# Optimization experiments

Measured on AMD Instinct MI355X. Metric: run time of the kernel, lower is better.

Reference implementation:

```python
import jax, jax.numpy as jnp
import numpy as np

HEADS = 16
D_MODEL = 1024
D_K = D_MODEL // HEADS
B, S = 2, 2048
NEG = -1000000000.0


def setup_inputs() -> dict:
    key = jax.random.key(0)
    ks = jax.random.split(key, 8)
    q = jax.random.normal(ks[0], (B, S, D_MODEL), dtype=jnp.float32)
    k = jax.random.normal(ks[1], (B, S, D_MODEL), dtype=jnp.float32)
    v = jax.random.normal(ks[2], (B, S, D_MODEL), dtype=jnp.float32)
    mask = jax.random.randint(ks[3], (B, 1, S, S), 0, 2) > 0  # True = masked
    scale = 1.0 / np.sqrt(D_MODEL)
    Wq = jax.random.normal(ks[4], (D_MODEL, D_MODEL), dtype=jnp.float32) * scale
    Wk = jax.random.normal(ks[5], (D_MODEL, D_MODEL), dtype=jnp.float32) * scale
    Wv = jax.random.normal(ks[6], (D_MODEL, D_MODEL), dtype=jnp.float32) * scale
    Wo = jax.random.normal(ks[7], (D_MODEL, D_MODEL), dtype=jnp.float32) * scale
    return {"q": q, "k": k, "v": v, "mask": mask,
            "Wq": Wq, "Wk": Wk, "Wv": Wv, "Wo": Wo}


def reference(q, k, v, mask, Wq, Wk, Wv, Wo):
    b, s, _ = q.shape
    # torch Linear: x @ W.T ; reshape to [B, H, S, d_k]
    def proj(x, W):
        return (x @ W.T).reshape(b, -1, HEADS, D_K).transpose(0, 2, 1, 3)
    qh, kh, vh = proj(q, Wq), proj(k, Wk), proj(v, Wv)
    # scaled dot-product attention; scale uses d_k (key.shape[-1] after reshape)
    att = jnp.einsum('bhqd,bhkd->bhqk', qh, kh) / jnp.sqrt(jnp.float32(D_K))
    att = jnp.where(mask, NEG, att)
    att = jax.nn.softmax(att, axis=-1)
    out = jnp.einsum('bhqk,bhkd->bhqd', att, vh)  # [B,H,S,d_k]
    out = out.transpose(0, 2, 1, 3).reshape(b, -1, D_MODEL)
    return out @ Wo.T  # dropout is identity at inference
```

## Files before the change

kernel.cpp:

```cpp
#include <hip/hip_runtime.h>

typedef unsigned short u16;
typedef unsigned int   u32;
typedef unsigned char  u8;
typedef unsigned long long u64;
typedef __attribute__((ext_vector_type(8))) short bf16x8;
typedef __attribute__((ext_vector_type(4))) float f32x4;
typedef __attribute__((ext_vector_type(16))) float f32x16;

__device__ __forceinline__ u16 f2b(float f) {
  union { float f; u32 u; } v; v.f = f;
  u32 u = v.u;
  return (u16)((u + 0x7fffu + ((u >> 16) & 1u)) >> 16);
}
__device__ __forceinline__ float b2f(u16 x) {
  union { u32 u; float f; } v; v.u = ((u32)x) << 16; return v.f;
}
__device__ __forceinline__ u32 pk2(u16 lo, u16 hi) { return (u32)lo | ((u32)hi << 16); }

__device__ __forceinline__ float fexp2(float x) { return __builtin_amdgcn_exp2f(x); }

__device__ __forceinline__ u32 cvtpk(float lo, float hi) {
  u32 r;
  asm("v_cvt_pk_bf16_f32 %0, %1, %2" : "=v"(r) : "v"(lo), "v"(hi));
  return r;
}

__device__ __forceinline__ void swap32(u32& a, u32& b) {
  asm("v_permlane32_swap_b32 %0, %1" : "+v"(a), "+v"(b));
}

__device__ __forceinline__ void glds16(const u16* g, u16* l) {
  __builtin_amdgcn_global_load_lds((const __attribute__((address_space(1))) void*)g,
                                   (__attribute__((address_space(3))) void*)l, 16, 0, 0);
}

__global__ __launch_bounds__(256) void mask_detect(const u8* __restrict__ raw,
                                                   int* __restrict__ flag) {
  int i = blockIdx.x * 256 + threadIdx.x;
  uint4 x = ((const uint4*)raw)[i];
  u32 o = x.x | x.y | x.z | x.w;
  u64 b1 = __ballot((o & 0x0000ff00u) != 0);
  u64 b2 = __ballot((o & 0xffff0000u) != 0);
  if ((threadIdx.x & 63) == 0) {
    if (b1) atomicOr(&flag[0], 1);
    if (b2) atomicOr(&flag[1], 1);
  }
}

__global__ __launch_bounds__(256) void mask_bits(const u8* __restrict__ raw,
                                                 u64* __restrict__ out,
                                                 const int* __restrict__ flag) {
  int f = flag[0] ? 2 : (flag[1] ? 1 : 0);
  int i = blockIdx.x * 256 + threadIdx.x;
  bool bit;
  if (f == 2)      bit = raw[i] != 0;
  else if (f == 0) bit = ((const int*)raw)[i] != 0;
  else             bit = ((const float*)raw)[i] != 0.0f;
  u64 b = __ballot(bit);
  if ((threadIdx.x & 63) == 0) out[i >> 6] = b;
}

__global__ __launch_bounds__(256) void conv_all(
    const float* __restrict__ W0, const float* __restrict__ W1,
    const float* __restrict__ W2, const float* __restrict__ W3,
    const float* __restrict__ A0, const float* __restrict__ A1,
    const float* __restrict__ A2,
    u16* __restrict__ o0, u16* __restrict__ o1, u16* __restrict__ o2,
    u16* __restrict__ o3, u16* __restrict__ o4, u16* __restrict__ o5,
    u16* __restrict__ o6) {
  int gid = blockIdx.x * 256 + threadIdx.x;
  const float* src; u16* dst; int off;
  if (gid < 524288) {
    int wz = gid >> 17; off = (gid & 131071) * 8;
    src = wz == 0 ? W0 : wz == 1 ? W1 : wz == 2 ? W2 : W3;
    dst = wz == 0 ? o0 : wz == 1 ? o1 : wz == 2 ? o2 : o3;
  } else {
    int g2 = gid - 524288;
    int az = g2 >> 19; off = (g2 & 524287) * 8;
    src = az == 0 ? A0 : az == 1 ? A1 : A2;
    dst = az == 0 ? o4 : az == 1 ? o5 : o6;
  }
  float4 a = *(const float4*)(src + off), b2 = *(const float4*)(src + off + 4);
  uint4 t;
  t.x = pk2(f2b(a.x), f2b(a.y));   t.y = pk2(f2b(a.z), f2b(a.w));
  t.z = pk2(f2b(b2.x), f2b(b2.y)); t.w = pk2(f2b(b2.z), f2b(b2.w));
  *(uint4*)(dst + off) = t;
}

template<int CF32>
__device__ __forceinline__ void gemm_body(
    const u16* __restrict__ Av, const u16* __restrict__ Bv, void* __restrict__ Cv,
    int N, int K, int m0, int n0, float cscale, u16* As, u16* Bs) {
  const int tid = threadIdx.x;
  const int lane = tid & 63, w = tid >> 6;
  const int lr = lane & 15, lg = lane >> 4;
  const int wm = (w >> 1) * 64, wn = (w & 1) * 64;
  const int srow = lane >> 3;
  const int selem = (((lane & 7) ^ srow) << 3);
  const int rsw = (lr & 7) << 3;

  f32x4 acc[4][4];
#pragma unroll
  for (int mi = 0; mi < 4; ++mi)
#pragma unroll
    for (int ni = 0; ni < 4; ++ni)
      acc[mi][ni] = (f32x4){0.f, 0.f, 0.f, 0.f};

#define GSTAGE(buf, k0_)                                                       \
  do {                                                                         \
    _Pragma("unroll")                                                          \
    for (int r_ = 0; r_ < 4; ++r_) {                                           \
      const int c_ = w * 4 + r_;                                               \
      const int row_ = c_ * 8 + srow;                                          \
      glds16(Av + (size_t)(m0 + row_) * K + (k0_) + selem, As + (buf) * 8192 + c_ * 512); \
      glds16(Bv + (size_t)(n0 + row_) * K + (k0_) + selem, Bs + (buf) * 8192 + c_ * 512); \
    }                                                                          \
  } while (0)

  GSTAGE(0, 0);
  __syncthreads();
  int cur = 0;
  for (int k0 = 0; k0 < K; k0 += 64) {
    if (k0 + 64 < K) GSTAGE(cur ^ 1, k0 + 64);
    bf16x8 af[4][2], bfv[4][2];
#pragma unroll
    for (int mi = 0; mi < 4; ++mi)
#pragma unroll
      for (int kk = 0; kk < 2; ++kk)
        af[mi][kk] = *(bf16x8*)&As[cur * 8192 + (wm + mi * 16 + lr) * 64 + ((kk * 32 + lg * 8) ^ rsw)];
#pragma unroll
    for (int ni = 0; ni < 4; ++ni)
#pragma unroll
      for (int kk = 0; kk < 2; ++kk)
        bfv[ni][kk] = *(bf16x8*)&Bs[cur * 8192 + (wn + ni * 16 + lr) * 64 + ((kk * 32 + lg * 8) ^ rsw)];
    __builtin_amdgcn_s_setprio(1);
#pragma unroll
    for (int mi = 0; mi < 4; ++mi)
#pragma unroll
      for (int ni = 0; ni < 4; ++ni)
#pragma unroll
        for (int kk = 0; kk < 2; ++kk)
          acc[mi][ni] = __builtin_amdgcn_mfma_f32_16x16x32_bf16(
              af[mi][kk], bfv[ni][kk], acc[mi][ni], 0, 0, 0);
    __builtin_amdgcn_s_setprio(0);
    __syncthreads();
    cur ^= 1;
  }
#undef GSTAGE
#pragma unroll
  for (int mi = 0; mi < 4; ++mi)
#pragma unroll
    for (int ni = 0; ni < 4; ++ni)
#pragma unroll
      for (int r = 0; r < 4; ++r) {
        int m = m0 + wm + mi * 16 + lg * 4 + r;
        int n = n0 + wn + ni * 16 + lr;
        float vv = acc[mi][ni][r] * cscale;
        if (CF32) ((float*)Cv)[(size_t)m * N + n] = vv;
        else      ((u16*)Cv)[(size_t)m * N + n] = f2b(vv);
      }
}

__global__ __launch_bounds__(256) void gemm_qkv(
    const u16* __restrict__ qb, const u16* __restrict__ kb, const u16* __restrict__ vb,
    const u16* __restrict__ Wqb, const u16* __restrict__ Wkb, const u16* __restrict__ Wvb,
    u16* __restrict__ Qb, u16* __restrict__ Kb, u16* __restrict__ VTb, float qscale) {
  __shared__ __align__(16) u16 As[2 * 8192];
  __shared__ __align__(16) u16 Bs[2 * 8192];
  const int z = blockIdx.z;
  const u16 *Av, *Bv; u16* Cv; int N, bxx, by; float cs = 1.0f;
  if (z < 2) {
    Av = z ? kb : qb; Bv = z ? Wkb : Wqb; Cv = z ? Kb : Qb;
    N = 1024; bxx = blockIdx.x & 7; by = blockIdx.x >> 3;
    if (!z) cs = qscale;
  } else {
    Av = Wvb; Bv = vb; Cv = VTb;
    N = 4096; bxx = blockIdx.x & 31; by = blockIdx.x >> 5;
  }
  gemm_body<0>(Av, Bv, Cv, N, 1024, by * 128, bxx * 128, cs, As, Bs);
}

__global__ __launch_bounds__(256) void gemm_o(
    const u16* __restrict__ Ob, const u16* __restrict__ Wob, float* __restrict__ C) {
  __shared__ __align__(16) u16 As[2 * 8192];
  __shared__ __align__(16) u16 Bs[2 * 8192];
  gemm_body<1>(Ob, Wob, C, 1024, 1024, blockIdx.y * 128, blockIdx.x * 128, 1.0f, As, Bs);
}

__global__ __launch_bounds__(256, 4) void flash12(const u16* __restrict__ Q,
                                                  const u16* __restrict__ K,
                                                  const u16* __restrict__ VT,
                                                  const u64* __restrict__ mpk,
                                                  u16* __restrict__ O0,
                                                  u16* __restrict__ O1,
                                                  u16* __restrict__ O2,
                                                  float* __restrict__ Lp) {
  __shared__ __align__(16) u16 Ks[2][4096];
  __shared__ __align__(16) u16 Vs[2][4096];
  const int tid = threadIdx.x, lane = tid & 63, w = tid >> 6;
  const int c = lane & 31, h = lane >> 5;
  const int bid = blockIdx.x;
  const int xcd = bid & 7, idx = bid >> 3;
  const int gl = idx >> 4, qblk = idx & 15;
  const int group = xcd * 12 + gl;
  const int split = group % 3;
  const int hb = group / 3;
  const int head = hb & 15, b = hb >> 4;
  const int qw = qblk * 128 + w * 32;
  const int kt0 = (split * 32) / 3;
  const int ktn = ((split + 1) * 32) / 3;
  const int nt = ktn - kt0;
  const size_t kbase = (size_t)b * 2048 * 1024 + (size_t)head * 64;
  const size_t vbase = (size_t)head * 64 * 4096 + (size_t)b * 2048;
  const int srow = lane >> 3;
  const int selem = (((lane & 7) ^ srow) << 3);
  const int rswc = (c & 7) << 3;

  bf16x8 qf[4];
#pragma unroll
  for (int kd = 0; kd < 4; ++kd)
    qf[kd] = *(const bf16x8*)&Q[kbase + (size_t)(qw + c) * 1024 + 16 * kd + 8 * h];

  union { u32 u[4]; bf16x8 v; } ones;
#pragma unroll
  for (int i = 0; i < 4; ++i) ones.u[i] = 0x3f803f80u;

  f32x16 accO0, accO1, accL;
#pragma unroll
  for (int i = 0; i < 16; ++i) { accO0[i] = 0.f; accO1[i] = 0.f; accL[i] = 0.f; }

  const u64* mrp = mpk + ((size_t)b * 2048 + qw + c) * 32;

#define STAGE(buf, t)                                                          \
  do {                                                                         \
    const int k0_ = (t) * 64;                                                  \
    _Pragma("unroll")                                                          \
    for (int r_ = 0; r_ < 2; ++r_) {                                           \
      const int c_ = w * 2 + r_;                                               \
      const int row_ = c_ * 8 + srow;                                          \
      glds16(K + kbase + (size_t)(k0_ + row_) * 1024 + selem, &Ks[buf][c_ * 512]); \
    }                                                                          \
    _Pragma("unroll")                                                          \
    for (int r_ = 0; r_ < 2; ++r_) {                                           \
      const int c_ = w * 2 + r_;                                               \
      const int row_ = c_ * 8 + srow;                                          \
      glds16(VT + vbase + (size_t)row_ * 4096 + k0_ + selem, &Vs[buf][c_ * 512]); \
    }                                                                          \
  } while (0)

  STAGE(0, kt0);
  u64 mb_next = mrp[kt0];
  __syncthreads();

  int cur = 0;
  for (int t = 0; t < nt; ++t) {
    const u64 mb = mb_next;
    if (t + 1 < nt) {
      STAGE(cur ^ 1, kt0 + t + 1);
      mb_next = mrp[kt0 + t + 1];
    }
    const u16* ks = Ks[cur];
    const u16* vs = Vs[cur];
    f32x16 s0, s1;
#pragma unroll
    for (int i = 0; i < 16; ++i) { s0[i] = 0.f; s1[i] = 0.f; }
    __builtin_amdgcn_s_setprio(1);
#pragma unroll
    for (int kd = 0; kd < 4; ++kd) {
      bf16x8 kf0 = *(bf16x8*)&ks[c * 64 + ((16 * kd + 8 * h) ^ rswc)];
      s0 = __builtin_amdgcn_mfma_f32_32x32x16_bf16(kf0, qf[kd], s0, 0, 0, 0);
      bf16x8 kf1 = *(bf16x8*)&ks[(32 + c) * 64 + ((16 * kd + 8 * h) ^ rswc)];
      s1 = __builtin_amdgcn_mfma_f32_32x32x16_bf16(kf1, qf[kd], s1, 0, 0, 0);
    }
    __builtin_amdgcn_s_setprio(0);
    u32 pw[2][4][2];
#pragma unroll
    for (int kb = 0; kb < 2; ++kb) {
      const u32 m32 = (u32)(mb >> (32 * kb + 4 * h));
      float pp[16];
#pragma unroll
      for (int g = 0; g < 4; ++g)
#pragma unroll
        for (int r = 0; r < 4; ++r) {
          float e = fexp2(kb == 0 ? s0[4 * g + r] : s1[4 * g + r]);
          pp[4 * g + r] = ((m32 >> (8 * g + r)) & 1) ? 0.0f : e;
        }
#pragma unroll
      for (int g = 0; g < 4; ++g)
#pragma unroll
        for (int hh = 0; hh < 2; ++hh)
          pw[kb][g][hh] = cvtpk(pp[4 * g + 2 * hh], pp[4 * g + 2 * hh + 1]);
    }
    __builtin_amdgcn_s_setprio(1);
#pragma unroll
    for (int kb = 0; kb < 2; ++kb)
#pragma unroll
      for (int s = 0; s < 2; ++s) {
        u32 w0 = pw[kb][2 * s][0], w2 = pw[kb][2 * s + 1][0];
        swap32(w0, w2);
        u32 w1 = pw[kb][2 * s][1], w3 = pw[kb][2 * s + 1][1];
        swap32(w1, w3);
        union { u32 u[4]; bf16x8 v; } af;
        af.u[0] = w0; af.u[1] = w1; af.u[2] = w2; af.u[3] = w3;
        const int ksg = kb * 2 + s;
        bf16x8 vf0 = *(bf16x8*)&vs[c * 64 + ((16 * ksg + 8 * h) ^ rswc)];
        accO0 = __builtin_amdgcn_mfma_f32_32x32x16_bf16(af.v, vf0, accO0, 0, 0, 0);
        bf16x8 vf1 = *(bf16x8*)&vs[(32 + c) * 64 + ((16 * ksg + 8 * h) ^ rswc)];
        accO1 = __builtin_amdgcn_mfma_f32_32x32x16_bf16(af.v, vf1, accO1, 0, 0, 0);
        accL  = __builtin_amdgcn_mfma_f32_32x32x16_bf16(af.v, ones.v, accL, 0, 0, 0);
      }
    __builtin_amdgcn_s_setprio(0);
    __syncthreads();
    cur ^= 1;
  }
#undef STAGE
  u16* Op = split == 0 ? O0 : split == 1 ? O1 : O2;
  const size_t obase = (size_t)b * 2048 + qw;
#pragma unroll
  for (int g = 0; g < 4; ++g)
#pragma unroll
    for (int r = 0; r < 4; ++r) {
      const int qrow = r + 8 * g + 4 * h;
      const size_t row = obase + qrow;
      const size_t base = row * 1024 + (size_t)head * 64 + c;
      Op[base]      = f2b(accO0[4 * g + r]);
      Op[base + 32] = f2b(accO1[4 * g + r]);
      if (c == 0) Lp[(size_t)split * 65536 + row * 16 + head] = accL[4 * g + r];
    }
}

__global__ __launch_bounds__(256) void combine(const u16* __restrict__ O0,
                                               const u16* __restrict__ O1,
                                               const u16* __restrict__ O2,
                                               const float* __restrict__ Lp,
                                               u16* __restrict__ Ob) {
  int gid = blockIdx.x * 256 + threadIdx.x;
  int row = gid >> 7, chb = (gid & 127) * 8;
  int head = chb >> 6;
  float l = Lp[(size_t)row * 16 + head] + Lp[65536 + (size_t)row * 16 + head] +
            Lp[131072 + (size_t)row * 16 + head];
  float inv = 1.0f / l;
  size_t off = (size_t)row * 1024 + chb;
  union { uint4 q; u16 s[8]; } a, b, c2, o;
  a.q  = *(const uint4*)(O0 + off);
  b.q  = *(const uint4*)(O1 + off);
  c2.q = *(const uint4*)(O2 + off);
#pragma unroll
  for (int j = 0; j < 8; ++j)
    o.s[j] = f2b((b2f(a.s[j]) + b2f(b.s[j]) + b2f(c2.s[j])) * inv);
  *(uint4*)(Ob + off) = o.q;
}

extern "C" void kernel_launch(void* const* d_in, const int* in_sizes, int n_in,
                              void* d_out, int out_size, void* d_ws, size_t ws_size,
                              hipStream_t stream) {
  const float* q    = (const float*)d_in[0];
  const float* k    = (const float*)d_in[1];
  const float* v    = (const float*)d_in[2];
  const u8*    mask = (const u8*)d_in[3];
  const float* Wq   = (const float*)d_in[4];
  const float* Wk   = (const float*)d_in[5];
  const float* Wv   = (const float*)d_in[6];
  const float* Wo   = (const float*)d_in[7];

  u8* ws = (u8*)d_ws;
  int* flag = (int*)ws;
  u64* mpk  = (u64*)(ws + 256);
  u16* Wqb  = (u16*)(ws + 256 + (1u << 20));
  u16* Wkb  = Wqb + (1 << 20);
  u16* Wvb  = Wkb + (1 << 20);
  u16* Wob  = Wvb + (1 << 20);
  const size_t NE = (size_t)4096 * 1024;
  u16* vb   = Wob + (1 << 20);
  u16* O2   = vb;
  u16* Qb   = vb + NE;
  u16* Kb   = Qb + NE;
  u16* VTb  = Kb + NE;
  u16* qb   = (u16*)d_out;
  u16* kb   = qb + NE;
  u16* O0   = qb;
  u16* O1   = kb;
  float* Lp = (float*)Wqb;
  u16* Ob   = Qb;

  const float LOG2E = 1.4426950408889634f;

  hipMemsetAsync(flag, 0, 8, stream);
  mask_detect<<<32, 256, 0, stream>>>(mask, flag);
  mask_bits<<<32768, 256, 0, stream>>>(mask, mpk, flag);
  conv_all<<<8192, 256, 0, stream>>>(Wq, Wk, Wv, Wo, q, k, v,
                                     Wqb, Wkb, Wvb, Wob, qb, kb, vb);

  gemm_qkv<<<dim3(256, 1, 3), 256, 0, stream>>>(
      qb, kb, vb, Wqb, Wkb, Wvb, Qb, Kb, VTb, 0.125f * LOG2E);

  flash12<<<1536, 256, 0, stream>>>(Qb, Kb, VTb, mpk, O0, O1, O2, Lp);
  combine<<<2048, 256, 0, stream>>>(O0, O1, O2, Lp, Ob);

  gemm_o<<<dim3(8, 32), 256, 0, stream>>>(Ob, Wob, (float*)d_out);
}
```

Measured before the change: 162.9 us.

## Vectorize mask packing, single-buffer QKV GEMM, XCD-remap grids, 128x64 output GEMM

mask_bits now has each thread read 8 mask elements and write one packed byte, instead of using a ballot per element, so it launches 8x fewer blocks. The QKV GEMM switches to single-buffered LDS so more blocks fit per CU, and block indices are remapped so blocks sharing an operand land on the same XCD for L2 reuse. The output GEMM uses 128x64 tiles to get 512 blocks instead of 256, for better CU fill. The cost is losing the overlap between loads and compute in the single-buffered loops.

```diff
diff --git a/kernel.cpp b/kernel.cpp
--- a/kernel.cpp
+++ b/kernel.cpp
@@ -52,13 +52,25 @@
                                                  u64* __restrict__ out,
                                                  const int* __restrict__ flag) {
   int f = flag[0] ? 2 : (flag[1] ? 1 : 0);
-  int i = blockIdx.x * 256 + threadIdx.x;
-  bool bit;
-  if (f == 2)      bit = raw[i] != 0;
-  else if (f == 0) bit = ((const int*)raw)[i] != 0;
-  else             bit = ((const float*)raw)[i] != 0.0f;
-  u64 b = __ballot(bit);
-  if ((threadIdx.x & 63) == 0) out[i >> 6] = b;
+  int t = blockIdx.x * 256 + threadIdx.x;
+  u8 byte;
+  if (f == 2) {
+    u64 x = ((const u64*)raw)[t];
+    u64 nz = x | (x >> 4); nz |= nz >> 2; nz |= nz >> 1;
+    nz &= 0x0101010101010101ull;
+    byte = (u8)((nz * 0x0102040810204080ull) >> 56);
+  } else if (f == 0) {
+    const int* ip = (const int*)raw + t * 8;
+    int4 a = *(const int4*)ip, b = *(const int4*)(ip + 4);
+    byte = (u8)((a.x != 0) | ((a.y != 0) << 1) | ((a.z != 0) << 2) | ((a.w != 0) << 3) |
+                ((b.x != 0) << 4) | ((b.y != 0) << 5) | ((b.z != 0) << 6) | ((b.w != 0) << 7));
+  } else {
+    const float* fp = (const float*)raw + t * 8;
+    float4 a = *(const float4*)fp, b = *(const float4*)(fp + 4);
+    byte = (u8)((a.x != 0.f) | ((a.y != 0.f) << 1) | ((a.z != 0.f) << 2) | ((a.w != 0.f) << 3) |
+                ((b.x != 0.f) << 4) | ((b.y != 0.f) << 5) | ((b.z != 0.f) << 6) | ((b.w != 0.f) << 7));
+  }
+  ((u8*)out)[t] = byte;
 }
 
 __global__ __launch_bounds__(256) void conv_all(
@@ -88,7 +100,7 @@
   *(uint4*)(dst + off) = t;
 }
 
-template<int CF32>
+template<int CF32, int DBUF>
 __device__ __forceinline__ void gemm_body(
     const u16* __restrict__ Av, const u16* __restrict__ Bv, void* __restrict__ Cv,
     int N, int K, int m0, int n0, float cscale, u16* As, u16* Bs) {
@@ -107,47 +119,62 @@
     for (int ni = 0; ni < 4; ++ni)
       acc[mi][ni] = (f32x4){0.f, 0.f, 0.f, 0.f};
 
-#define GSTAGE(buf, k0_)                                                       \
+#define GLDS2(k0_, LA, LB)                                                     \
   do {                                                                         \
     _Pragma("unroll")                                                          \
     for (int r_ = 0; r_ < 4; ++r_) {                                           \
       const int c_ = w * 4 + r_;                                               \
       const int row_ = c_ * 8 + srow;                                          \
-      glds16(Av + (size_t)(m0 + row_) * K + (k0_) + selem, As + (buf) * 8192 + c_ * 512); \
-      glds16(Bv + (size_t)(n0 + row_) * K + (k0_) + selem, Bs + (buf) * 8192 + c_ * 512); \
+      glds16(Av + (size_t)(m0 + row_) * K + (k0_) + selem, (LA) + c_ * 512);   \
+      glds16(Bv + (size_t)(n0 + row_) * K + (k0_) + selem, (LB) + c_ * 512);   \
     }                                                                          \
   } while (0)
 
-  GSTAGE(0, 0);
-  __syncthreads();
-  int cur = 0;
-  for (int k0 = 0; k0 < K; k0 += 64) {
-    if (k0 + 64 < K) GSTAGE(cur ^ 1, k0 + 64);
-    bf16x8 af[4][2], bfv[4][2];
-#pragma unroll
-    for (int mi = 0; mi < 4; ++mi)
-#pragma unroll
-      for (int kk = 0; kk < 2; ++kk)
-        af[mi][kk] = *(bf16x8*)&As[cur * 8192 + (wm + mi * 16 + lr) * 64 + ((kk * 32 + lg * 8) ^ rsw)];
-#pragma unroll
-    for (int ni = 0; ni < 4; ++ni)
-#pragma unroll
-      for (int kk = 0; kk < 2; ++kk)
-        bfv[ni][kk] = *(bf16x8*)&Bs[cur * 8192 + (wn + ni * 16 + lr) * 64 + ((kk * 32 + lg * 8) ^ rsw)];
-    __builtin_amdgcn_s_setprio(1);
-#pragma unroll
-    for (int mi = 0; mi < 4; ++mi)
-#pragma unroll
-      for (int ni = 0; ni < 4; ++ni)
-#pragma unroll
-        for (int kk = 0; kk < 2; ++kk)
-          acc[mi][ni] = __builtin_amdgcn_mfma_f32_16x16x32_bf16(
-              af[mi][kk], bfv[ni][kk], acc[mi][ni], 0, 0, 0);
-    __builtin_amdgcn_s_setprio(0);
+#define FRAG_MFMA(bufA, bufB)                                                  \
+  do {                                                                         \
+    bf16x8 af[4][2], bfv[4][2];                                                \
+    _Pragma("unroll")                                                          \
+    for (int mi = 0; mi < 4; ++mi)                                             \
+      _Pragma("unroll")                                                        \
+      for (int kk = 0; kk < 2; ++kk)                                           \
+        af[mi][kk] = *(bf16x8*)&(bufA)[(wm + mi * 16 + lr) * 64 + ((kk * 32 + lg * 8) ^ rsw)]; \
+    _Pragma("unroll")                                                          \
+    for (int ni = 0; ni < 4; ++ni)                                             \
+      _Pragma("unroll")                                                        \
+      for (int kk = 0; kk < 2; ++kk)                                           \
+        bfv[ni][kk] = *(bf16x8*)&(bufB)[(wn + ni * 16 + lr) * 64 + ((kk * 32 + lg * 8) ^ rsw)]; \
+    __builtin_amdgcn_s_setprio(1);                                             \
+    _Pragma("unroll")                                                          \
+    for (int mi = 0; mi < 4; ++mi)                                             \
+      _Pragma("unroll")                                                        \
+      for (int ni = 0; ni < 4; ++ni)                                           \
+        _Pragma("unroll")                                                      \
+        for (int kk = 0; kk < 2; ++kk)                                         \
+          acc[mi][ni] = __builtin_amdgcn_mfma_f32_16x16x32_bf16(               \
+              af[mi][kk], bfv[ni][kk], acc[mi][ni], 0, 0, 0);                  \
+    __builtin_amdgcn_s_setprio(0);                                             \
+  } while (0)
+
+  if (DBUF) {
+    GLDS2(0, As, Bs);
     __syncthreads();
-    cur ^= 1;
-  }
-#undef GSTAGE
+    int cur = 0;
+    for (int k0 = 0; k0 < K; k0 += 64) {
+      if (k0 + 64 < K) GLDS2(k0 + 64, As + (cur ^ 1) * 8192, Bs + (cur ^ 1) * 8192);
+      FRAG_MFMA(As + cur * 8192, Bs + cur * 8192);
+      __syncthreads();
+      cur ^= 1;
+    }
+  } else {
+    for (int k0 = 0; k0 < K; k0 += 64) {
+      __syncthreads();
+      GLDS2(k0, As, Bs);
+      __syncthreads();
+      FRAG_MFMA(As, Bs);
+    }
+  }
+#undef GLDS2
+#undef FRAG_MFMA
 #pragma unroll
   for (int mi = 0; mi < 4; ++mi)
 #pragma unroll
@@ -166,26 +193,97 @@
     const u16* __restrict__ qb, const u16* __restrict__ kb, const u16* __restrict__ vb,
     const u16* __restrict__ Wqb, const u16* __restrict__ Wkb, const u16* __restrict__ Wvb,
     u16* __restrict__ Qb, u16* __restrict__ Kb, u16* __restrict__ VTb, float qscale) {
-  __shared__ __align__(16) u16 As[2 * 8192];
-  __shared__ __align__(16) u16 Bs[2 * 8192];
+  __shared__ __align__(16) u16 As[8192];
+  __shared__ __align__(16) u16 Bs[8192];
   const int z = blockIdx.z;
-  const u16 *Av, *Bv; u16* Cv; int N, bxx, by; float cs = 1.0f;
+  const int xcd = blockIdx.x & 7, r = blockIdx.x >> 3;
+  const int pblk = xcd * 4 + (r & 3);
+  const int oblk = r >> 2;
   if (z < 2) {
-    Av = z ? kb : qb; Bv = z ? Wkb : Wqb; Cv = z ? Kb : Qb;
-    N = 1024; bxx = blockIdx.x & 7; by = blockIdx.x >> 3;
-    if (!z) cs = qscale;
+    const u16* act = z ? kb : qb;
+    const u16* Wb = z ? Wkb : Wqb;
+    u16* Cb = z ? Kb : Qb;
+    gemm_body<0, 0>(act, Wb, Cb, 1024, 1024, pblk * 128, oblk * 128,
+                    z ? 1.0f : qscale, As, Bs);
   } else {
-    Av = Wvb; Bv = vb; Cv = VTb;
-    N = 4096; bxx = blockIdx.x & 31; by = blockIdx.x >> 5;
-  }
-  gemm_body<0>(Av, Bv, Cv, N, 1024, by * 128, bxx * 128, cs, As, Bs);
+    gemm_body<0, 0>(Wvb, vb, VTb, 4096, 1024, oblk * 128, pblk * 128, 1.0f, As, Bs);
+  }
+}
+
+__device__ __forceinline__ void gemm64_body(
+    const u16* __restrict__ Av, const u16* __restrict__ Bv, float* __restrict__ Cv,
+    int N, int K, int m0, int n0, u16* As, u16* Bs) {
+  const int tid = threadIdx.x;
+  const int lane = tid & 63, w = tid >> 6;
+  const int lr = lane & 15, lg = lane >> 4;
+  const int wm = w * 32;
+  const int srow = lane >> 3;
+  const int selem = (((lane & 7) ^ srow) << 3);
+  const int rsw = (lr & 7) << 3;
+
+  f32x4 acc[2][4];
+#pragma unroll
+  for (int mi = 0; mi < 2; ++mi)
+#pragma unroll
+    for (int ni = 0; ni < 4; ++ni)
+      acc[mi][ni] = (f32x4){0.f, 0.f, 0.f, 0.f};
+
+  for (int k0 = 0; k0 < K; k0 += 64) {
+    __syncthreads();
+#pragma unroll
+    for (int r_ = 0; r_ < 4; ++r_) {
+      const int c_ = w * 4 + r_;
+      const int row_ = c_ * 8 + srow;
+      glds16(Av + (size_t)(m0 + row_) * K + k0 + selem, As + c_ * 512);
+    }
+#pragma unroll
+    for (int r_ = 0; r_ < 2; ++r_) {
+      const int c_ = w * 2 + r_;
+      const int row_ = c_ * 8 + srow;
+      glds16(Bv + (size_t)(n0 + row_) * K + k0 + selem, Bs + c_ * 512);
+    }
+    __syncthreads();
+    bf16x8 af[2][2], bfv[4][2];
+#pragma unroll
+    for (int mi = 0; mi < 2; ++mi)
+#pragma unroll
+      for (int kk = 0; kk < 2; ++kk)
+        af[mi][kk] = *(bf16x8*)&As[(wm + mi * 16 + lr) * 64 + ((kk * 32 + lg * 8) ^ rsw)];
+#pragma unroll
+    for (int ni = 0; ni < 4; ++ni)
+#pragma unroll
+      for (int kk = 0; kk < 2; ++kk)
+        bfv[ni][kk] = *(bf16x8*)&Bs[(ni * 16 + lr) * 64 + ((kk * 32 + lg * 8) ^ rsw)];
+    __builtin_amdgcn_s_setprio(1);
+#pragma unroll
+    for (int mi = 0; mi < 2; ++mi)
+#pragma unroll
+      for (int ni = 0; ni < 4; ++ni)
+#pragma unroll
+        for (int kk = 0; kk < 2; ++kk)
+          acc[mi][ni] = __builtin_amdgcn_mfma_f32_16x16x32_bf16(
+              af[mi][kk], bfv[ni][kk], acc[mi][ni], 0, 0, 0);
+    __builtin_amdgcn_s_setprio(0);
+  }
+#pragma unroll
+  for (int mi = 0; mi < 2; ++mi)
+#pragma unroll
+    for (int ni = 0; ni < 4; ++ni)
+#pragma unroll
+      for (int r = 0; r < 4; ++r) {
+        int m = m0 + wm + mi * 16 + lg * 4 + r;
+        int n = n0 + ni * 16 + lr;
+        Cv[(size_t)m * N + n] = acc[mi][ni][r];
+      }
 }
 
 __global__ __launch_bounds__(256) void gemm_o(
     const u16* __restrict__ Ob, const u16* __restrict__ Wob, float* __restrict__ C) {
-  __shared__ __align__(16) u16 As[2 * 8192];
-  __shared__ __align__(16) u16 Bs[2 * 8192];
-  gemm_body<1>(Ob, Wob, C, 1024, 1024, blockIdx.y * 128, blockIdx.x * 128, 1.0f, As, Bs);
+  __shared__ __align__(16) u16 As[128 * 64];
+  __shared__ __align__(16) u16 Bs[64 * 64];
+  const int xcd = blockIdx.x & 7, r = blockIdx.x >> 3;
+  const int mblk = xcd * 4 + (r & 3), nblk = r >> 2;
+  gemm64_body(Ob, Wob, C, 1024, 1024, mblk * 128, nblk * 64, As, Bs);
 }
 
 __global__ __launch_bounds__(256, 4) void flash12(const u16* __restrict__ Q,
@@ -388,7 +486,7 @@
 
   hipMemsetAsync(flag, 0, 8, stream);
   mask_detect<<<32, 256, 0, stream>>>(mask, flag);
-  mask_bits<<<32768, 256, 0, stream>>>(mask, mpk, flag);
+  mask_bits<<<4096, 256, 0, stream>>>(mask, mpk, flag);
   conv_all<<<8192, 256, 0, stream>>>(Wq, Wk, Wv, Wo, q, k, v,
                                      Wqb, Wkb, Wvb, Wob, qb, kb, vb);
 
@@ -398,5 +496,5 @@
   flash12<<<1536, 256, 0, stream>>>(Qb, Kb, VTb, mpk, O0, O1, O2, Lp);
   combine<<<2048, 256, 0, stream>>>(O0, O1, O2, Lp, Ob);
 
-  gemm_o<<<dim3(8, 32), 256, 0, stream>>>(Ob, Wob, (float*)d_out);
-}
+  gemm_o<<<512, 256, 0, stream>>>(Ob, Wob, (float*)d_out);
+}
```

Result: faster. 142.7 us (-12.4%).
